# Kernel optimization log

Measured on AMD Instinct MI355X. Metric: run time of the kernel, lower is better.

The kernel has to match this reference:

```python
import jax, jax.numpy as jnp
import numpy as np

D_MODEL = 1024
BLOCK_SIZE = 2048


def setup_inputs() -> dict:
    key = jax.random.key(0)
    ks = jax.random.split(key, 9)
    B, T, C = 4, 2048, D_MODEL
    s = 1.0 / np.sqrt(C)
    return {
        "x": jax.random.normal(ks[0], (B, T, C), dtype=jnp.float32),
        "Wq": jax.random.normal(ks[1], (C, C), dtype=jnp.float32) * s,
        "bq": jnp.zeros((C,), dtype=jnp.float32),
        "Wk": jax.random.normal(ks[2], (C, C), dtype=jnp.float32) * s,
        "bk": jnp.zeros((C,), dtype=jnp.float32),
        "Wv": jax.random.normal(ks[3], (C, C), dtype=jnp.float32) * s,
        "bv": jnp.zeros((C,), dtype=jnp.float32),
        "Wo": jax.random.normal(ks[4], (C, C), dtype=jnp.float32) * s,
        "bo": jnp.zeros((C,), dtype=jnp.float32),
    }


def reference(x, Wq, bq, Wk, bk, Wv, bv, Wo, bo):
    B, T, C = x.shape
    q = x @ Wq + bq
    k = x @ Wk + bk
    v = x @ Wv + bv
    # NOTE: original module never splits heads; attention is over full d_model
    score = jnp.einsum("btc,bsc->bts", q, k) / jnp.sqrt(jnp.asarray(C, x.dtype))
    causal = jnp.tril(jnp.ones((T, T), dtype=bool))
    score = jnp.where(causal, score, jnp.asarray(-jnp.inf, x.dtype))
    probs = jax.nn.softmax(score, axis=-1)
    out = jnp.einsum("bts,bsc->btc", probs, v)
    return out @ Wo + bo
```

## Files before the change

### kernel.cpp

```cpp
#include <hip/hip_runtime.h>
#include <hip/hip_bf16.h>
#include <stdint.h>


typedef __attribute__((ext_vector_type(8))) __bf16 bf16x8;
typedef __attribute__((ext_vector_type(4))) __bf16 bf16x4;
typedef __attribute__((ext_vector_type(4))) float f32x4;

#define MFMA16(A, B, C) __builtin_amdgcn_mfma_f32_16x16x32_bf16(A, B, C, 0, 0, 0)
#define BAR() asm volatile("s_barrier" ::: "memory")

#define T_SEQ 2048
#define D_MOD 1024

static __device__ __forceinline__ void gload_lds16(const void* g, void* l) {
  __builtin_amdgcn_global_load_lds(
      (const __attribute__((address_space(1))) void*)g,
      (__attribute__((address_space(3))) void*)l, 16, 0, 0);
}

__global__ void cvt_bf16_kernel(const float* __restrict__ in,
                                __bf16* __restrict__ out, int n8) {
  int i = blockIdx.x * blockDim.x + threadIdx.x;
  if (i < n8) {
    const float4* p = (const float4*)(in + (size_t)i * 8);
    float4 a = p[0], b = p[1];
    bf16x8 o;
    o[0] = (__bf16)a.x; o[1] = (__bf16)a.y; o[2] = (__bf16)a.z; o[3] = (__bf16)a.w;
    o[4] = (__bf16)b.x; o[5] = (__bf16)b.y; o[6] = (__bf16)b.z; o[7] = (__bf16)b.w;
    *(bf16x8*)(out + (size_t)i * 8) = o;
  }
}

__global__ void transpose_cvt4_kernel(const float* __restrict__ Wq,
                                      const float* __restrict__ Wk,
                                      const float* __restrict__ Wv,
                                      const float* __restrict__ Wo,
                                      __bf16* __restrict__ Wqkvt,
                                      __bf16* __restrict__ Wot) {
  __shared__ float tile[32][33];
  const int z = blockIdx.z;
  const float* W = (z == 0) ? Wq : (z == 1) ? Wk : (z == 2) ? Wv : Wo;
  __bf16* Wt = (z < 3) ? (Wqkvt + (size_t)z * 1024 * 1024) : Wot;
  int tx = threadIdx.x, ty = threadIdx.y;
  int bx = blockIdx.x * 32, by = blockIdx.y * 32;
#pragma unroll
  for (int i = 0; i < 4; i++)
    tile[ty + 8 * i][tx] = W[(size_t)(by + ty + 8 * i) * D_MOD + bx + tx];
  __syncthreads();
#pragma unroll
  for (int i = 0; i < 4; i++)
    Wt[(size_t)(bx + ty + 8 * i) * D_MOD + by + tx] = (__bf16)tile[tx][ty + 8 * i];
}

__global__ __launch_bounds__(512, 2) void qkv384_kernel(
    const __bf16* __restrict__ A, const __bf16* __restrict__ Bt,
    const float* __restrict__ bq, const float* __restrict__ bk,
    const float* __restrict__ bv, __bf16* __restrict__ Qo,
    __bf16* __restrict__ Ko, __bf16* __restrict__ Vto) {
  constexpr int NT = 16;
  __shared__ __align__(16) char lds[131072];
#define ABUF(p) (lds + (p) * 16384)
#define BBUF(p) (lds + 32768 + (p) * 49152)

  const int tid = threadIdx.x;
  const int w = tid >> 6, l = tid & 63;
  const int wr = w >> 2, wc = w & 3;
  const int cpx = gridDim.x >> 3;
  const int swz = ((int)blockIdx.x & 7) * cpx + ((int)blockIdx.x >> 3);
  const int bm = (swz >> 3) * 128;
  const int bn = (swz & 7) * 384;

  const int cswz = (l & 3) ^ ((l >> 3) & 3);
  const int rlo = l & 15;
  const int xsw = (((l >> 4) ^ ((l >> 1) & 3)) << 4);

#define STAGE_A(t, p)                                                     \
  {                                                                       \
    const __bf16* g = A + (size_t)(bm + w * 16 + (l >> 2)) * 1024 +       \
                      (t) * 64 + cswz * 8;                                \
    char* d = ABUF(p) + w * 1024 + l * 16;                                \
    gload_lds16(g, d);                                                    \
    gload_lds16(g + 32, d + 8192);                                        \
  }
#define STAGE_B(t, p, gch)                                                \
  {                                                                       \
    const __bf16* g = Bt +                                                \
        (size_t)(bn + ((gch) * 8 + w) * 16 + (l >> 2)) * 1024 +           \
        (t) * 64 + cswz * 8;                                              \
    char* d = BBUF(p) + ((gch) * 8 + w) * 1024 + l * 16;                  \
    gload_lds16(g, d);                                                    \
    gload_lds16(g + 32, d + 24576);                                       \
  }
#define LDA_FRAG(p, i, kk)                                        \
  (*(const bf16x8*)(ABUF(p) + (kk) * 8192 +                       \
                    (wr * 64 + (i) * 16 + rlo) * 64 + xsw))
#define LDB_FRAG(p, gch, n, kk)                                   \
  (*(const bf16x8*)(BBUF(p) + (kk) * 24576 +                      \
                    (wc * 96 + (gch) * 32 + (n) * 16 + rlo) * 64 + xsw))

  f32x4 acc[4][6] = {};
  STAGE_A(0, 0);
  STAGE_B(0, 0, 0); STAGE_B(0, 0, 1); STAGE_B(0, 0, 2);
  STAGE_A(1, 1);
  asm volatile("s_waitcnt vmcnt(2)" ::: "memory");
  BAR();

  for (int t = 0; t < NT; ++t) {
    const int p = t & 1;
    bf16x8 a[4][2], bfr[2][2];
#pragma unroll
    for (int i = 0; i < 4; i++) {
      a[i][0] = LDA_FRAG(p, i, 0);
      a[i][1] = LDA_FRAG(p, i, 1);
    }
#pragma unroll
    for (int n = 0; n < 2; n++) {
      bfr[n][0] = LDB_FRAG(p, 0, n, 0);
      bfr[n][1] = LDB_FRAG(p, 0, n, 1);
    }
    if (t + 1 < NT) {
      STAGE_B(t + 1, p ^ 1, 0);
      STAGE_B(t + 1, p ^ 1, 1);
      STAGE_B(t + 1, p ^ 1, 2);
    }
    BAR();
    __builtin_amdgcn_s_setprio(1);
#pragma unroll
    for (int i = 0; i < 4; i++)
#pragma unroll
      for (int n = 0; n < 2; n++) {
        acc[i][n] = MFMA16(a[i][0], bfr[n][0], acc[i][n]);
        acc[i][n] = MFMA16(a[i][1], bfr[n][1], acc[i][n]);
      }
    __builtin_amdgcn_s_setprio(0);
    BAR();
#pragma unroll
    for (int n = 0; n < 2; n++) {
      bfr[n][0] = LDB_FRAG(p, 1, n, 0);
      bfr[n][1] = LDB_FRAG(p, 1, n, 1);
    }
    if (t + 2 < NT) STAGE_A(t + 2, p);
    BAR();
    __builtin_amdgcn_s_setprio(1);
#pragma unroll
    for (int i = 0; i < 4; i++)
#pragma unroll
      for (int n = 0; n < 2; n++) {
        acc[i][2 + n] = MFMA16(a[i][0], bfr[n][0], acc[i][2 + n]);
        acc[i][2 + n] = MFMA16(a[i][1], bfr[n][1], acc[i][2 + n]);
      }
    __builtin_amdgcn_s_setprio(0);
    BAR();
#pragma unroll
    for (int n = 0; n < 2; n++) {
      bfr[n][0] = LDB_FRAG(p, 2, n, 0);
      bfr[n][1] = LDB_FRAG(p, 2, n, 1);
    }
    BAR();
    __builtin_amdgcn_s_setprio(1);
#pragma unroll
    for (int i = 0; i < 4; i++)
#pragma unroll
      for (int n = 0; n < 2; n++) {
        acc[i][4 + n] = MFMA16(a[i][0], bfr[n][0], acc[i][4 + n]);
        acc[i][4 + n] = MFMA16(a[i][1], bfr[n][1], acc[i][4 + n]);
      }
    __builtin_amdgcn_s_setprio(0);
    if (t < NT - 2) asm volatile("s_waitcnt vmcnt(2)" ::: "memory");
    else asm volatile("s_waitcnt vmcnt(0)" ::: "memory");
    BAR();
  }

  const int l4 = (l >> 4) * 4;
#pragma unroll
  for (int gch = 0; gch < 3; gch++)
#pragma unroll
    for (int n = 0; n < 2; n++) {
      const int cbase = bn + wc * 96 + gch * 32 + n * 16;
      const int seg = cbase >> 10;
      const int lcol = (cbase & 1023) + rlo;
      const int an = gch * 2 + n;
      if (seg < 2) {
        const float* bs = seg ? bk : bq;
        __bf16* os = seg ? Ko : Qo;
        const float bvv = bs[lcol];
#pragma unroll
        for (int i = 0; i < 4; i++) {
          const int rowb = bm + wr * 64 + i * 16 + l4;
#pragma unroll
          for (int r = 0; r < 4; r++)
            os[(size_t)(rowb + r) * D_MOD + lcol] =
                (__bf16)(acc[i][an][r] + bvv);
        }
      } else {
        const float bvv = bv[lcol];
#pragma unroll
        for (int i = 0; i < 4; i++) {
          const int rowb = bm + wr * 64 + i * 16 + l4;
          const int z = rowb >> 11, tt = rowb & 2047;
          bf16x4 pk;
#pragma unroll
          for (int r = 0; r < 4; r++) pk[r] = (__bf16)(acc[i][an][r] + bvv);
          *(bf16x4*)(Vto + (size_t)z * (D_MOD * T_SEQ) +
                     (size_t)lcol * T_SEQ + tt) = pk;
        }
      }
    }
#undef ABUF
#undef BBUF
#undef STAGE_A
#undef STAGE_B
#undef LDA_FRAG
#undef LDB_FRAG
}

template <int MG, int NG>
static __device__ __forceinline__ void mfma_quad(f32x4 (&acc)[8][4],
                                                 const bf16x8 (&aR)[4][2],
                                                 const bf16x8 (&bR)[2][2]) {
#pragma unroll
  for (int i = 0; i < 4; i++)
#pragma unroll
    for (int n = 0; n < 2; n++)
#pragma unroll
      for (int kk = 0; kk < 2; kk++)
        acc[MG * 4 + i][NG * 2 + n] =
            MFMA16(aR[i][kk], bR[n][kk], acc[MG * 4 + i][NG * 2 + n]);
}

__global__ __launch_bounds__(512, 2) void qk_kernel(
    const __bf16* __restrict__ A, const __bf16* __restrict__ Bt,
    float* __restrict__ So, size_t bsA, size_t bsB, size_t bsC) {
  constexpr int NT = 16;
  __shared__ __align__(16) char lds[131072];
#define ABUF(p, h) (lds + ((p) * 2 + (h)) * 16384)
#define BBUF(p, h) (lds + 65536 + ((p) * 2 + (h)) * 16384)

  const int tid = threadIdx.x;
  const int w = tid >> 6, l = tid & 63;
  const int wr = w >> 2, wc = w & 3;
  if ((int)blockIdx.y > (int)blockIdx.x) return;
  const int bm = blockIdx.x * 256, bn = blockIdx.y * 256;
  const int z = blockIdx.z;
  A += (size_t)z * bsA;
  Bt += (size_t)z * bsB;

  const int grow = l >> 2;
  const int cswz = (l & 3) ^ ((l >> 3) & 3);
  const int rlo = l & 15;
  const int xsw = (((l >> 4) ^ ((l >> 1) & 3)) << 4);

#define STAGE_A(t, h)                                                       \
  {                                                                         \
    const __bf16* g = A + (size_t)(bm + (h) * 128 + w * 16 + grow) * 1024 + \
                      (t) * 64 + cswz * 8;                                  \
    char* d = ABUF((t) & 1, h) + w * 1024 + l * 16;                         \
    gload_lds16(g, d);                                                      \
    gload_lds16(g + 32, d + 8192);                                          \
  }
#define STAGE_B(t, h)                                                       \
  {                                                                         \
    const __bf16* g = Bt + (size_t)(bn + (h) * 128 + w * 16 + grow) * 1024 +\
                      (t) * 64 + cswz * 8;                                  \
    char* d = BBUF((t) & 1, h) + w * 1024 + l * 16;                         \
    gload_lds16(g, d);                                                      \
    gload_lds16(g + 32, d + 8192);                                          \
  }
#define LDA_FRAG(p, g, i, kk)                                     \
  (*(const bf16x8*)(ABUF(p, wr) + (kk) * 8192 +                   \
                    ((g) * 64 + (i) * 16 + rlo) * 64 + xsw))
#define LDB_FRAG(p, g, n, kk)                                     \
  (*(const bf16x8*)(BBUF(p, (wc >> 1)) + (kk) * 8192 +            \
                    ((wc & 1) * 64 + (g) * 32 + (n) * 16 + rlo) * 64 + xsw))

  f32x4 acc[8][4] = {};
  STAGE_A(0, 0); STAGE_A(0, 1);
  STAGE_B(0, 0); STAGE_B(0, 1);
  STAGE_A(1, 0); STAGE_A(1, 1);
  asm volatile("s_waitcnt vmcnt(4)" ::: "memory");
  BAR();

  for (int t = 0; t < NT; ++t) {
    const int p = t & 1;
    bf16x8 a[4][2], b[2][2];
#pragma unroll
    for (int i = 0; i < 4; i++) {
      a[i][0] = LDA_FRAG(p, 0, i, 0);
      a[i][1] = LDA_FRAG(p, 0, i, 1);
    }
#pragma unroll
    for (int n = 0; n < 2; n++) {
      b[n][0] = LDB_FRAG(p, 0, n, 0);
      b[n][1] = LDB_FRAG(p, 0, n, 1);
    }
    if (t + 1 < NT) STAGE_B(t + 1, 0);
    BAR();
    __builtin_amdgcn_s_setprio(1);
    mfma_quad<0, 0>(acc, a, b);
    __builtin_amdgcn_s_setprio(0);
    BAR();
    bf16x8 b2[2][2];
#pragma unroll
    for (int n = 0; n < 2; n++) {
      b2[n][0] = LDB_FRAG(p, 1, n, 0);
      b2[n][1] = LDB_FRAG(p, 1, n, 1);
    }
    if (t + 1 < NT) STAGE_B(t + 1, 1);
    BAR();
    __builtin_amdgcn_s_setprio(1);
    mfma_quad<0, 1>(acc, a, b2);
    __builtin_amdgcn_s_setprio(0);
    BAR();
#pragma unroll
    for (int i = 0; i < 4; i++) {
      a[i][0] = LDA_FRAG(p, 1, i, 0);
      a[i][1] = LDA_FRAG(p, 1, i, 1);
    }
    BAR();
    __builtin_amdgcn_s_setprio(1);
    mfma_quad<1, 1>(acc, a, b2);
    __builtin_amdgcn_s_setprio(0);
    BAR();
#pragma unroll
    for (int n = 0; n < 2; n++) {
      b[n][0] = LDB_FRAG(p, 0, n, 0);
      b[n][1] = LDB_FRAG(p, 0, n, 1);
    }
    if (t + 2 < NT) {
      STAGE_A(t + 2, 0); STAGE_A(t + 2, 1);
      BAR();
      __builtin_amdgcn_s_setprio(1);
      mfma_quad<1, 0>(acc, a, b);
      __builtin_amdgcn_s_setprio(0);
      asm volatile("s_waitcnt vmcnt(4)" ::: "memory");
      BAR();
    } else {
      BAR();
      __builtin_amdgcn_s_setprio(1);
      mfma_quad<1, 0>(acc, a, b);
      __builtin_amdgcn_s_setprio(0);
      asm volatile("s_waitcnt vmcnt(0)" ::: "memory");
      BAR();
    }
  }

  float* os = So + (size_t)z * bsC;
#pragma unroll
  for (int n4 = 0; n4 < 4; n4++) {
    int col = bn + wc * 64 + n4 * 16 + rlo;
#pragma unroll
    for (int mi = 0; mi < 8; mi++) {
      int rowb = bm + wr * 128 + mi * 16 + (l >> 4) * 4;
#pragma unroll
      for (int r = 0; r < 4; r++) {
        int row = rowb + r;
        float v = acc[mi][n4][r] * 0.03125f;
        if (col > row) v = -1e30f;
        os[(size_t)row * T_SEQ + col] = v;
      }
    }
  }
#undef ABUF
#undef BBUF
#undef STAGE_A
#undef STAGE_B
#undef LDA_FRAG
#undef LDB_FRAG
}

template <int MODE>
__global__ __launch_bounds__(512, 2) void ugemm_kernel(
    const __bf16* __restrict__ A, const __bf16* __restrict__ Bt,
    const float* __restrict__ b0, void* __restrict__ o0, int lda, int ldb,
    size_t bsA, size_t bsB, size_t bsC) {
  __shared__ __align__(16) char lds[147456];
#define ABUF(p3) (lds + (p3) * 16384)
#define BBUF(p3) (lds + 49152 + (p3) * 32768)

  const int tid = threadIdx.x;
  const int w = tid >> 6, l = tid & 63;
  const int wr = w >> 2, wc = w & 3;
  const int z = blockIdx.z;

  int bm, bn, NT;
  if (MODE == 1) {
    const int cpx = gridDim.x >> 3;
    const int swz = ((int)blockIdx.x & 7) * cpx + ((int)blockIdx.x >> 3);
    bm = (swz >> 2) * 128; bn = (swz & 3) * 256; NT = 16;
  } else {
    const int i = (int)blockIdx.x >> 2;
    bm = i * 128; bn = ((int)blockIdx.x & 3) * 256; NT = (i + 1) * 2;
  }
  A += (size_t)z * bsA;
  Bt += (size_t)z * bsB;

  const int grow = w * 16 + (l >> 2);
  const int cswz = (l & 3) ^ ((l >> 3) & 3);
  const int rlo = l & 15;
  const int xsw = (((l >> 4) ^ ((l >> 1) & 3)) << 4);

#define STAGE_A(t, p3)                                                       \
  {                                                                          \
    const __bf16* g = A + (size_t)(bm + grow) * lda + (t) * 64 + cswz * 8;   \
    char* d = ABUF(p3) + w * 1024 + l * 16;                                  \
    gload_lds16(g, d);                                                       \
    gload_lds16(g + 32, d + 8192);                                           \
  }
#define STAGE_B(t, p3)                                                       \
  {                                                                          \
    const __bf16* g = Bt + (size_t)(bn + grow) * ldb + (t) * 64 + cswz * 8;  \
    char* d = BBUF(p3) + w * 1024 + l * 16;                                  \
    gload_lds16(g, d);                                                       \
    gload_lds16(g + 32, d + 16384);                                          \
    const __bf16* g2 = g + (size_t)128 * ldb;                                \
    gload_lds16(g2, d + 8192);                                               \
    gload_lds16(g2 + 32, d + 8192 + 16384);                                  \
  }
#define LDA_FRAG(p3, i, kk)                                       \
  (*(const bf16x8*)(ABUF(p3) + (kk) * 8192 +                      \
                    (wr * 64 + (i) * 16 + rlo) * 64 + xsw))
#define LDB_FRAG(p3, n, kk)                                       \
  (*(const bf16x8*)(BBUF(p3) + (kk) * 16384 +                     \
                    (wc * 64 + (n) * 16 + rlo) * 64 + xsw))

  f32x4 acc[4][4] = {};
  STAGE_A(0, 0); STAGE_B(0, 0);
  STAGE_A(1, 1); STAGE_B(1, 1);
  asm volatile("s_waitcnt vmcnt(6)" ::: "memory");
  BAR();

  int p = 0, pn2 = 2;
  for (int t = 0; t < NT; ++t) {
    bf16x8 af[4][2], bf01[2][2], bf23[2][2];
#pragma unroll
    for (int i = 0; i < 4; i++) {
      af[i][0] = LDA_FRAG(p, i, 0);
      af[i][1] = LDA_FRAG(p, i, 1);
    }
#pragma unroll
    for (int n = 0; n < 2; n++) {
      bf01[n][0] = LDB_FRAG(p, n, 0);
      bf01[n][1] = LDB_FRAG(p, n, 1);
    }
    if (t + 2 < NT) STAGE_A(t + 2, pn2);
    BAR();
    __builtin_amdgcn_s_setprio(1);
#pragma unroll
    for (int i = 0; i < 4; i++)
#pragma unroll
      for (int n = 0; n < 2; n++) {
        acc[i][n] = MFMA16(af[i][0], bf01[n][0], acc[i][n]);
        acc[i][n] = MFMA16(af[i][1], bf01[n][1], acc[i][n]);
      }
    __builtin_amdgcn_s_setprio(0);
    BAR();
#pragma unroll
    for (int n = 0; n < 2; n++) {
      bf23[n][0] = LDB_FRAG(p, n + 2, 0);
      bf23[n][1] = LDB_FRAG(p, n + 2, 1);
    }
    if (t + 2 < NT) STAGE_B(t + 2, pn2);
    BAR();
    __builtin_amdgcn_s_setprio(1);
#pragma unroll
    for (int i = 0; i < 4; i++)
#pragma unroll
      for (int n = 0; n < 2; n++) {
        acc[i][n + 2] = MFMA16(af[i][0], bf23[n][0], acc[i][n + 2]);
        acc[i][n + 2] = MFMA16(af[i][1], bf23[n][1], acc[i][n + 2]);
      }
    __builtin_amdgcn_s_setprio(0);
    if (t + 2 < NT) {
      asm volatile("s_waitcnt vmcnt(6)" ::: "memory");
    } else {
      asm volatile("s_waitcnt vmcnt(0)" ::: "memory");
    }
    BAR();
    p = (p + 1 == 3) ? 0 : p + 1;
    pn2 = (pn2 + 1 == 3) ? 0 : pn2 + 1;
  }

  if (MODE == 1) {
    float* os = (float*)o0;
#pragma unroll
    for (int n = 0; n < 4; n++) {
      int col = bn + wc * 64 + n * 16 + rlo;
      float bvv = b0[col];
#pragma unroll
      for (int m = 0; m < 4; m++) {
        int rowb = bm + wr * 64 + m * 16 + (l >> 4) * 4;
#pragma unroll
        for (int r = 0; r < 4; r++)
          os[(size_t)(rowb + r) * D_MOD + col] = acc[m][n][r] + bvv;
      }
    }
  } else {
    __bf16* os = (__bf16*)o0 + (size_t)z * bsC;
#pragma unroll
    for (int n = 0; n < 4; n++) {
      int col = bn + wc * 64 + n * 16 + rlo;
#pragma unroll
      for (int m = 0; m < 4; m++) {
        int rowb = bm + wr * 64 + m * 16 + (l >> 4) * 4;
#pragma unroll
        for (int r = 0; r < 4; r++)
          os[(size_t)(rowb + r) * D_MOD + col] = (__bf16)acc[m][n][r];
      }
    }
  }
#undef ABUF
#undef BBUF
#undef STAGE_A
#undef STAGE_B
#undef LDA_FRAG
#undef LDB_FRAG
}

__global__ __launch_bounds__(256) void softmax_kernel(float* __restrict__ S,
                                                      size_t bstride) {
  const int t = blockIdx.x, b = blockIdx.y;
  float* Srow = S + (size_t)b * bstride + (size_t)t * T_SEQ;
  __bf16* Prow = (__bf16*)Srow;
  const int L = ((t + 1) + 127) & ~127;
  const int tid = threadIdx.x;
  const int base = tid * 8;
  const bool act = base < L;
  float v[8];
  float m = -1e30f;
  if (act) {
    float4 a = *(const float4*)(Srow + base);
    float4 c = *(const float4*)(Srow + base + 4);
    v[0] = a.x; v[1] = a.y; v[2] = a.z; v[3] = a.w;
    v[4] = c.x; v[5] = c.y; v[6] = c.z; v[7] = c.w;
#pragma unroll
    for (int j = 0; j < 8; j++) m = fmaxf(m, v[j]);
  }
#pragma unroll
  for (int off = 1; off < 64; off <<= 1) m = fmaxf(m, __shfl_xor(m, off));
  __shared__ float redm[4], reds[4];
  const int wave = tid >> 6, lane = tid & 63;
  if (lane == 0) redm[wave] = m;
  __syncthreads();
  m = fmaxf(fmaxf(redm[0], redm[1]), fmaxf(redm[2], redm[3]));
  float p[8];
  float s = 0.f;
  if (act) {
#pragma unroll
    for (int j = 0; j < 8; j++) {
      p[j] = __expf(v[j] - m);
      s += p[j];
    }
  }
#pragma unroll
  for (int off = 1; off < 64; off <<= 1) s += __shfl_xor(s, off);
  if (lane == 0) reds[wave] = s;
  __syncthreads();
  const float inv = 1.0f / (reds[0] + reds[1] + reds[2] + reds[3]);
  if (act) {
    bf16x8 o;
#pragma unroll
    for (int j = 0; j < 8; j++) o[j] = (__bf16)(p[j] * inv);
    *(bf16x8*)(Prow + base) = o;
  }
}

extern "C" void kernel_launch(void* const* d_in, const int* in_sizes, int n_in,
                              void* d_out, int out_size, void* d_ws,
                              size_t ws_size, hipStream_t stream) {
  const float* x = (const float*)d_in[0];
  const float* Wq = (const float*)d_in[1];
  const float* bq = (const float*)d_in[2];
  const float* Wk = (const float*)d_in[3];
  const float* bk = (const float*)d_in[4];
  const float* Wv = (const float*)d_in[5];
  const float* bv = (const float*)d_in[6];
  const float* Wo = (const float*)d_in[7];
  const float* bo = (const float*)d_in[8];

  char* ws = (char*)d_ws;
  const size_t MB = 1u << 20;
  const size_t TC = (size_t)T_SEQ * D_MOD;
  const size_t TT = (size_t)T_SEQ * T_SEQ;
  __bf16* xb    = (__bf16*)(ws);
  __bf16* Wqkvt = (__bf16*)(ws + 16 * MB);
  __bf16* Wot   = (__bf16*)(ws + 22 * MB);
  __bf16* Qb    = (__bf16*)(ws + 24 * MB);
  __bf16* Kb    = (__bf16*)(ws + 40 * MB);
  __bf16* Vtb   = (__bf16*)(ws + 56 * MB);

  cvt_bf16_kernel<<<4096, 256, 0, stream>>>(x, xb, 8192 * D_MOD / 8);
  transpose_cvt4_kernel<<<dim3(32, 32, 4), dim3(32, 8), 0, stream>>>(
      Wq, Wk, Wv, Wo, Wqkvt, Wot);
  qkv384_kernel<<<512, 512, 0, stream>>>(xb, Wqkvt, bq, bk, bv, Qb, Kb, Vtb);

  const bool batched = ws_size >= 137 * MB;
  if (batched) {
    float* S = (float*)(ws + 72 * MB);
    __bf16* AO = Qb;
    qk_kernel<<<dim3(8, 8, 4), 512, 0, stream>>>(Qb, Kb, S, TC, TC, TT);
    softmax_kernel<<<dim3(T_SEQ, 4), 256, 0, stream>>>(S, TT);
    ugemm_kernel<2><<<dim3(64, 1, 4), 512, 0, stream>>>(
        (const __bf16*)S, Vtb, nullptr, AO, 2 * T_SEQ, T_SEQ, TT * 2, TC, TC);
    ugemm_kernel<1><<<256, 512, 0, stream>>>(AO, Wot, bo, d_out, D_MOD, D_MOD,
                                             0, 0, 0);
  } else {
    float* S = (float*)(ws);
    __bf16* AO = Qb;
    for (int b = 0; b < 4; ++b) {
      qk_kernel<<<dim3(8, 8, 1), 512, 0, stream>>>(Qb + b * TC, Kb + b * TC, S,
                                                   0, 0, 0);
      softmax_kernel<<<dim3(T_SEQ, 1), 256, 0, stream>>>(S, 0);
      ugemm_kernel<2><<<dim3(64, 1, 1), 512, 0, stream>>>(
          (const __bf16*)S, Vtb + b * TC, nullptr, AO + b * TC, 2 * T_SEQ,
          T_SEQ, 0, 0, 0);
    }
    ugemm_kernel<1><<<256, 512, 0, stream>>>(AO, Wot, bo, d_out, D_MOD, D_MOD,
                                             0, 0, 0);
  }
}
```

Measured before the change: 185.5 us.

## Software-pipeline QKV GEMM fragments and load-balance causal PV GEMM with paired tiles

The QKV projection loop now prefetches the next k-tile's A and B0 fragments into registers and issues B loads two stages ahead, with fewer barriers per iteration, so LDS reads overlap the MFMA work. The PV GEMM gets its own kernel: 128-column tiles, and each block handles a causal row tile together with its mirror (i and 15-i), so every block does the same total work instead of the triangular imbalance. The output projection is split into a dedicated kernel with constant strides. The cost is higher register pressure from the double-buffered fragments, plus sequential segments per block in the PV kernel.

```diff
diff --git a/kernel.cpp b/kernel.cpp
--- a/kernel.cpp
+++ b/kernel.cpp
@@ -100,76 +100,97 @@
                     (wc * 96 + (gch) * 32 + (n) * 16 + rlo) * 64 + xsw))
 
   f32x4 acc[4][6] = {};
+  bf16x8 a_c[4][2], a_n[4][2], b0_c[2][2], b0_n[2][2], b1f[2][2], b2f[2][2];
+
   STAGE_A(0, 0);
   STAGE_B(0, 0, 0); STAGE_B(0, 0, 1); STAGE_B(0, 0, 2);
   STAGE_A(1, 1);
-  asm volatile("s_waitcnt vmcnt(2)" ::: "memory");
+  STAGE_B(1, 1, 0); STAGE_B(1, 1, 1); STAGE_B(1, 1, 2);
+  asm volatile("s_waitcnt vmcnt(8)" ::: "memory");
   BAR();
+#pragma unroll
+  for (int i = 0; i < 4; i++) {
+    a_c[i][0] = LDA_FRAG(0, i, 0);
+    a_c[i][1] = LDA_FRAG(0, i, 1);
+  }
+#pragma unroll
+  for (int n = 0; n < 2; n++) {
+    b0_c[n][0] = LDB_FRAG(0, 0, n, 0);
+    b0_c[n][1] = LDB_FRAG(0, 0, n, 1);
+  }
 
   for (int t = 0; t < NT; ++t) {
     const int p = t & 1;
-    bf16x8 a[4][2], bfr[2][2];
-#pragma unroll
-    for (int i = 0; i < 4; i++) {
-      a[i][0] = LDA_FRAG(p, i, 0);
-      a[i][1] = LDA_FRAG(p, i, 1);
-    }
-#pragma unroll
-    for (int n = 0; n < 2; n++) {
-      bfr[n][0] = LDB_FRAG(p, 0, n, 0);
-      bfr[n][1] = LDB_FRAG(p, 0, n, 1);
-    }
+#pragma unroll
+    for (int n = 0; n < 2; n++) {
+      b1f[n][0] = LDB_FRAG(p, 1, n, 0);
+      b1f[n][1] = LDB_FRAG(p, 1, n, 1);
+    }
+    __builtin_amdgcn_s_setprio(1);
+#pragma unroll
+    for (int i = 0; i < 4; i++)
+#pragma unroll
+      for (int n = 0; n < 2; n++) {
+        acc[i][n] = MFMA16(a_c[i][0], b0_c[n][0], acc[i][n]);
+        acc[i][n] = MFMA16(a_c[i][1], b0_c[n][1], acc[i][n]);
+      }
+    __builtin_amdgcn_s_setprio(0);
+    BAR();
+#pragma unroll
+    for (int n = 0; n < 2; n++) {
+      b2f[n][0] = LDB_FRAG(p, 2, n, 0);
+      b2f[n][1] = LDB_FRAG(p, 2, n, 1);
+    }
+    if (t + 2 < NT) STAGE_A(t + 2, p);
+    __builtin_amdgcn_s_setprio(1);
+#pragma unroll
+    for (int i = 0; i < 4; i++)
+#pragma unroll
+      for (int n = 0; n < 2; n++) {
+        acc[i][2 + n] = MFMA16(a_c[i][0], b1f[n][0], acc[i][2 + n]);
+        acc[i][2 + n] = MFMA16(a_c[i][1], b1f[n][1], acc[i][2 + n]);
+      }
+    __builtin_amdgcn_s_setprio(0);
+    if (t + 2 < NT) asm volatile("s_waitcnt vmcnt(2)" ::: "memory");
+    else asm volatile("s_waitcnt vmcnt(0)" ::: "memory");
+    BAR();
     if (t + 1 < NT) {
-      STAGE_B(t + 1, p ^ 1, 0);
-      STAGE_B(t + 1, p ^ 1, 1);
-      STAGE_B(t + 1, p ^ 1, 2);
-    }
-    BAR();
+#pragma unroll
+      for (int i = 0; i < 4; i++) {
+        a_n[i][0] = LDA_FRAG(p ^ 1, i, 0);
+        a_n[i][1] = LDA_FRAG(p ^ 1, i, 1);
+      }
+#pragma unroll
+      for (int n = 0; n < 2; n++) {
+        b0_n[n][0] = LDB_FRAG(p ^ 1, 0, n, 0);
+        b0_n[n][1] = LDB_FRAG(p ^ 1, 0, n, 1);
+      }
+    }
+    if (t + 2 < NT) {
+      STAGE_B(t + 2, p, 0); STAGE_B(t + 2, p, 1); STAGE_B(t + 2, p, 2);
+    }
     __builtin_amdgcn_s_setprio(1);
 #pragma unroll
     for (int i = 0; i < 4; i++)
 #pragma unroll
       for (int n = 0; n < 2; n++) {
-        acc[i][n] = MFMA16(a[i][0], bfr[n][0], acc[i][n]);
-        acc[i][n] = MFMA16(a[i][1], bfr[n][1], acc[i][n]);
+        acc[i][4 + n] = MFMA16(a_c[i][0], b2f[n][0], acc[i][4 + n]);
+        acc[i][4 + n] = MFMA16(a_c[i][1], b2f[n][1], acc[i][4 + n]);
       }
     __builtin_amdgcn_s_setprio(0);
     BAR();
-#pragma unroll
-    for (int n = 0; n < 2; n++) {
-      bfr[n][0] = LDB_FRAG(p, 1, n, 0);
-      bfr[n][1] = LDB_FRAG(p, 1, n, 1);
-    }
-    if (t + 2 < NT) STAGE_A(t + 2, p);
-    BAR();
-    __builtin_amdgcn_s_setprio(1);
-#pragma unroll
-    for (int i = 0; i < 4; i++)
+    if (t + 1 < NT) {
+#pragma unroll
+      for (int i = 0; i < 4; i++) {
+        a_c[i][0] = a_n[i][0];
+        a_c[i][1] = a_n[i][1];
+      }
 #pragma unroll
       for (int n = 0; n < 2; n++) {
-        acc[i][2 + n] = MFMA16(a[i][0], bfr[n][0], acc[i][2 + n]);
-        acc[i][2 + n] = MFMA16(a[i][1], bfr[n][1], acc[i][2 + n]);
-      }
-    __builtin_amdgcn_s_setprio(0);
-    BAR();
-#pragma unroll
-    for (int n = 0; n < 2; n++) {
-      bfr[n][0] = LDB_FRAG(p, 2, n, 0);
-      bfr[n][1] = LDB_FRAG(p, 2, n, 1);
-    }
-    BAR();
-    __builtin_amdgcn_s_setprio(1);
-#pragma unroll
-    for (int i = 0; i < 4; i++)
-#pragma unroll
-      for (int n = 0; n < 2; n++) {
-        acc[i][4 + n] = MFMA16(a[i][0], bfr[n][0], acc[i][4 + n]);
-        acc[i][4 + n] = MFMA16(a[i][1], bfr[n][1], acc[i][4 + n]);
-      }
-    __builtin_amdgcn_s_setprio(0);
-    if (t < NT - 2) asm volatile("s_waitcnt vmcnt(2)" ::: "memory");
-    else asm volatile("s_waitcnt vmcnt(0)" ::: "memory");
-    BAR();
+        b0_c[n][0] = b0_n[n][0];
+        b0_c[n][1] = b0_n[n][1];
+      }
+    }
   }
 
   const int l4 = (l >> 4) * 4;
@@ -369,51 +390,147 @@
 #undef LDB_FRAG
 }
 
-template <int MODE>
-__global__ __launch_bounds__(512, 2) void ugemm_kernel(
-    const __bf16* __restrict__ A, const __bf16* __restrict__ Bt,
-    const float* __restrict__ b0, void* __restrict__ o0, int lda, int ldb,
-    size_t bsA, size_t bsB, size_t bsC) {
-  __shared__ __align__(16) char lds[147456];
+__global__ __launch_bounds__(512, 2) void pv_kernel(
+    const __bf16* __restrict__ Ap, const __bf16* __restrict__ Btp,
+    __bf16* __restrict__ Op, size_t bsA, size_t bsB, size_t bsC) {
+  __shared__ __align__(16) char lds[98304];
 #define ABUF(p3) (lds + (p3) * 16384)
-#define BBUF(p3) (lds + 49152 + (p3) * 32768)
+#define BBUF(p3) (lds + 49152 + (p3) * 16384)
 
   const int tid = threadIdx.x;
   const int w = tid >> 6, l = tid & 63;
   const int wr = w >> 2, wc = w & 3;
+  const int pid = (int)blockIdx.x >> 3;
+  const int bn = ((int)blockIdx.x & 7) * 128;
   const int z = blockIdx.z;
-
-  int bm, bn, NT;
-  if (MODE == 1) {
-    const int cpx = gridDim.x >> 3;
-    const int swz = ((int)blockIdx.x & 7) * cpx + ((int)blockIdx.x >> 3);
-    bm = (swz >> 2) * 128; bn = (swz & 3) * 256; NT = 16;
-  } else {
-    const int i = (int)blockIdx.x >> 2;
-    bm = i * 128; bn = ((int)blockIdx.x & 3) * 256; NT = (i + 1) * 2;
-  }
-  A += (size_t)z * bsA;
-  Bt += (size_t)z * bsB;
+  const __bf16* A = Ap + (size_t)z * bsA;
+  const __bf16* Bt = Btp + (size_t)z * bsB;
+  __bf16* O = Op + (size_t)z * bsC;
 
   const int grow = w * 16 + (l >> 2);
   const int cswz = (l & 3) ^ ((l >> 3) & 3);
   const int rlo = l & 15;
   const int xsw = (((l >> 4) ^ ((l >> 1) & 3)) << 4);
 
-#define STAGE_A(t, p3)                                                       \
+#define PSTAGE_A(t, p3)                                                      \
   {                                                                          \
-    const __bf16* g = A + (size_t)(bm + grow) * lda + (t) * 64 + cswz * 8;   \
+    const __bf16* g = A + (size_t)(bm + grow) * 4096 + (t) * 64 + cswz * 8;  \
     char* d = ABUF(p3) + w * 1024 + l * 16;                                  \
     gload_lds16(g, d);                                                       \
     gload_lds16(g + 32, d + 8192);                                           \
   }
+#define PSTAGE_B(t, p3)                                                      \
+  {                                                                          \
+    const __bf16* g = Bt + (size_t)(bn + grow) * 2048 + (t) * 64 + cswz * 8; \
+    char* d = BBUF(p3) + w * 1024 + l * 16;                                  \
+    gload_lds16(g, d);                                                       \
+    gload_lds16(g + 32, d + 8192);                                           \
+  }
+#define PLDA(p3, i, kk)                                           \
+  (*(const bf16x8*)(ABUF(p3) + (kk) * 8192 +                      \
+                    (wr * 64 + (i) * 16 + rlo) * 64 + xsw))
+#define PLDB(p3, n, kk)                                           \
+  (*(const bf16x8*)(BBUF(p3) + (kk) * 8192 +                      \
+                    (wc * 32 + (n) * 16 + rlo) * 64 + xsw))
+
+#pragma unroll
+  for (int seg = 0; seg < 2; ++seg) {
+    const int i = seg ? (15 - pid) : pid;
+    const int bm = i * 128;
+    const int NT = (i + 1) * 2;
+    f32x4 acc[4][2] = {};
+
+    PSTAGE_A(0, 0); PSTAGE_B(0, 0);
+    if (NT > 1) { PSTAGE_A(1, 1); PSTAGE_B(1, 1); }
+    asm volatile("s_waitcnt vmcnt(4)" ::: "memory");
+    BAR();
+
+    int p = 0, pn2 = 2;
+    for (int t = 0; t < NT; ++t) {
+      bf16x8 af[4][2], bfv[2][2];
+#pragma unroll
+      for (int m = 0; m < 4; m++) {
+        af[m][0] = PLDA(p, m, 0);
+        af[m][1] = PLDA(p, m, 1);
+      }
+#pragma unroll
+      for (int n = 0; n < 2; n++) {
+        bfv[n][0] = PLDB(p, n, 0);
+        bfv[n][1] = PLDB(p, n, 1);
+      }
+      if (t + 2 < NT) { PSTAGE_A(t + 2, pn2); PSTAGE_B(t + 2, pn2); }
+      BAR();
+      __builtin_amdgcn_s_setprio(1);
+#pragma unroll
+      for (int m = 0; m < 4; m++)
+#pragma unroll
+        for (int n = 0; n < 2; n++) {
+          acc[m][n] = MFMA16(af[m][0], bfv[n][0], acc[m][n]);
+          acc[m][n] = MFMA16(af[m][1], bfv[n][1], acc[m][n]);
+        }
+      __builtin_amdgcn_s_setprio(0);
+      if (t + 2 < NT) asm volatile("s_waitcnt vmcnt(4)" ::: "memory");
+      else asm volatile("s_waitcnt vmcnt(0)" ::: "memory");
+      BAR();
+      p = (p + 1 == 3) ? 0 : p + 1;
+      pn2 = (pn2 + 1 == 3) ? 0 : pn2 + 1;
+    }
+
+#pragma unroll
+    for (int n = 0; n < 2; n++) {
+      int col = bn + wc * 32 + n * 16 + rlo;
+#pragma unroll
+      for (int m = 0; m < 4; m++) {
+        int rowb = bm + wr * 64 + m * 16 + (l >> 4) * 4;
+#pragma unroll
+        for (int r = 0; r < 4; r++)
+          O[(size_t)(rowb + r) * D_MOD + col] = (__bf16)acc[m][n][r];
+      }
+    }
+    BAR();
+  }
+#undef ABUF
+#undef BBUF
+#undef PSTAGE_A
+#undef PSTAGE_B
+#undef PLDA
+#undef PLDB
+}
+
+__global__ __launch_bounds__(512, 2) void oproj_kernel(
+    const __bf16* __restrict__ A, const __bf16* __restrict__ Bt,
+    const float* __restrict__ b0, float* __restrict__ o0) {
+  constexpr int NT = 16;
+  __shared__ __align__(16) char lds[147456];
+#define ABUF(p3) (lds + (p3) * 16384)
+#define BBUF(p3) (lds + 49152 + (p3) * 32768)
+
+  const int tid = threadIdx.x;
+  const int w = tid >> 6, l = tid & 63;
+  const int wr = w >> 2, wc = w & 3;
+  const int cpx = gridDim.x >> 3;
+  const int swz = ((int)blockIdx.x & 7) * cpx + ((int)blockIdx.x >> 3);
+  const int bm = (swz >> 2) * 128, bn = (swz & 3) * 256;
+
+  const int grow = w * 16 + (l >> 2);
+  const int cswz = (l & 3) ^ ((l >> 3) & 3);
+  const int rlo = l & 15;
+  const int xsw = (((l >> 4) ^ ((l >> 1) & 3)) << 4);
+
+#define STAGE_A(t, p3)                                                       \
+  {                                                                          \
+    const __bf16* g = A + (size_t)(bm + grow) * 1024 + (t) * 64 + cswz * 8;  \
+    char* d = ABUF(p3) + w * 1024 + l * 16;                                  \
+    gload_lds16(g, d);                                                       \
+    gload_lds16(g + 32, d + 8192);                                           \
+  }
 #define STAGE_B(t, p3)                                                       \
   {                                                                          \
-    const __bf16* g = Bt + (size_t)(bn + grow) * ldb + (t) * 64 + cswz * 8;  \
+    const __bf16* g = Bt + (size_t)(bn + grow) * 1024 + (t) * 64 + cswz * 8; \
     char* d = BBUF(p3) + w * 1024 + l * 16;                                  \
     gload_lds16(g, d);                                                       \
     gload_lds16(g + 32, d + 16384);                                          \
-    const __bf16* g2 = g + (size_t)128 * ldb;                                \
+    const __bf16* g2 = g + (size_t)128 * 1024;                               \
     gload_lds16(g2, d + 8192);                                               \
     gload_lds16(g2 + 32, d + 8192 + 16384);                                  \
   }
@@ -481,32 +598,16 @@
     pn2 = (pn2 + 1 == 3) ? 0 : pn2 + 1;
   }
 
-  if (MODE == 1) {
-    float* os = (float*)o0;
-#pragma unroll
-    for (int n = 0; n < 4; n++) {
-      int col = bn + wc * 64 + n * 16 + rlo;
-      float bvv = b0[col];
-#pragma unroll
-      for (int m = 0; m < 4; m++) {
-        int rowb = bm + wr * 64 + m * 16 + (l >> 4) * 4;
-#pragma unroll
-        for (int r = 0; r < 4; r++)
-          os[(size_t)(rowb + r) * D_MOD + col] = acc[m][n][r] + bvv;
-      }
-    }
-  } else {
-    __bf16* os = (__bf16*)o0 + (size_t)z * bsC;
-#pragma unroll
-    for (int n = 0; n < 4; n++) {
-      int col = bn + wc * 64 + n * 16 + rlo;
-#pragma unroll
-      for (int m = 0; m < 4; m++) {
-        int rowb = bm + wr * 64 + m * 16 + (l >> 4) * 4;
-#pragma unroll
-        for (int r = 0; r < 4; r++)
-          os[(size_t)(rowb + r) * D_MOD + col] = (__bf16)acc[m][n][r];
-      }
+#pragma unroll
+  for (int n = 0; n < 4; n++) {
+    int col = bn + wc * 64 + n * 16 + rlo;
+    float bvv = b0[col];
+#pragma unroll
+    for (int m = 0; m < 4; m++) {
+      int rowb = bm + wr * 64 + m * 16 + (l >> 4) * 4;
+#pragma unroll
+      for (int r = 0; r < 4; r++)
+        o0[(size_t)(rowb + r) * D_MOD + col] = acc[m][n][r] + bvv;
     }
   }
 #undef ABUF
@@ -600,10 +701,9 @@
     __bf16* AO = Qb;
     qk_kernel<<<dim3(8, 8, 4), 512, 0, stream>>>(Qb, Kb, S, TC, TC, TT);
     softmax_kernel<<<dim3(T_SEQ, 4), 256, 0, stream>>>(S, TT);
-    ugemm_kernel<2><<<dim3(64, 1, 4), 512, 0, stream>>>(
-        (const __bf16*)S, Vtb, nullptr, AO, 2 * T_SEQ, T_SEQ, TT * 2, TC, TC);
-    ugemm_kernel<1><<<256, 512, 0, stream>>>(AO, Wot, bo, d_out, D_MOD, D_MOD,
-                                             0, 0, 0);
+    pv_kernel<<<dim3(64, 1, 4), 512, 0, stream>>>((const __bf16*)S, Vtb, AO,
+                                                  TT * 2, TC, TC);
+    oproj_kernel<<<256, 512, 0, stream>>>(AO, Wot, bo, (float*)d_out);
   } else {
     float* S = (float*)(ws);
     __bf16* AO = Qb;
@@ -611,11 +711,9 @@
       qk_kernel<<<dim3(8, 8, 1), 512, 0, stream>>>(Qb + b * TC, Kb + b * TC, S,
                                                    0, 0, 0);
       softmax_kernel<<<dim3(T_SEQ, 1), 256, 0, stream>>>(S, 0);
-      ugemm_kernel<2><<<dim3(64, 1, 1), 512, 0, stream>>>(
-          (const __bf16*)S, Vtb + b * TC, nullptr, AO + b * TC, 2 * T_SEQ,
-          T_SEQ, 0, 0, 0);
-    }
-    ugemm_kernel<1><<<256, 512, 0, stream>>>(AO, Wot, bo, d_out, D_MOD, D_MOD,
-                                             0, 0, 0);
-  }
-}
+      pv_kernel<<<dim3(64, 1, 1), 512, 0, stream>>>(
+          (const __bf16*)S, Vtb + b * TC, AO + b * TC, 0, 0, 0);
+    }
+    oproj_kernel<<<256, 512, 0, stream>>>(AO, Wot, bo, (float*)d_out);
+  }
+}
```

After: 175.1 us. 1.06x faster.
